# Performance work log

Hardware: AMD Instinct MI355X
Metric: run time of the kernel (lower is better)

Reference implementation:

```python
import math
import jax, jax.numpy as jnp
import numpy as np

T, C, NH = 2048, 1024, 16
HD = C // NH


def setup_inputs() -> dict:
    key = jax.random.key(0)
    ks = jax.random.split(key, 5)
    return {
        "x": jax.random.normal(ks[0], (T, C), dtype=jnp.float32),
        "w_attn": jax.random.normal(ks[1], (3 * C, C), dtype=jnp.float32) * (1.0 / math.sqrt(C)),
        "b_attn": jax.random.normal(ks[2], (3 * C,), dtype=jnp.float32) * 0.02,
        "w_proj": jax.random.normal(ks[3], (C, C), dtype=jnp.float32) * (1.0 / math.sqrt(C)),
        "b_proj": jax.random.normal(ks[4], (C,), dtype=jnp.float32) * 0.02,
    }


def reference(x, w_attn, b_attn, w_proj, b_proj):
    t, c = x.shape
    # qkv projection: eqx Linear computes W @ x + b, vmapped over T
    qkv = x @ w_attn.T + b_attn  # (T, 3C)
    q, k, v = jnp.split(qkv, 3, axis=1)  # each (T, C)
    # (T, NH, HD) -> (NH, T, HD)
    q = jnp.swapaxes(q.reshape(t, NH, HD), 0, 1)
    k = jnp.swapaxes(k.reshape(t, NH, HD), 0, 1)
    v = jnp.swapaxes(v.reshape(t, NH, HD), 0, 1)
    att = jnp.einsum('hqd,hkd->hqk', q, k) / math.sqrt(HD)  # (NH, T, T)
    causal = jnp.tril(jnp.ones((t, t), dtype=bool))
    att = jnp.where(causal[None, :, :], att, -jnp.inf)
    att = jax.nn.softmax(att, axis=-1)
    y = jnp.matmul(att, v)  # (NH, T, HD)
    # Faithful to source: swapaxes(1,2) on (NH, T, HD) -> (NH, HD, T), then reshape
    y = jnp.swapaxes(y, 1, 2).reshape(t, c)
    return y @ w_proj.T + b_proj
```

## Files before the change

### kernel.cpp

```cpp
#include <hip/hip_runtime.h>
#include <hip/hip_bf16.h>
#include <stdint.h>

typedef __bf16 bf16;
typedef __bf16 bf16x8 __attribute__((ext_vector_type(8)));
typedef __bf16 bf16x4 __attribute__((ext_vector_type(4)));
typedef float floatx4 __attribute__((ext_vector_type(4)));

#define T_DIM 2048
#define C_DIM 1024
#define NH    16
#define HD    64

__device__ __forceinline__ void gload_lds16(const void* g, void* l) {
    __builtin_amdgcn_global_load_lds(
        (__attribute__((address_space(1))) void*)(g),
        (__attribute__((address_space(3))) void*)(l),
        16, 0, 0);
}

#define MFMA16(a, b, c) __builtin_amdgcn_mfma_f32_16x16x32_bf16(a, b, c, 0, 0, 0)

__global__ __launch_bounds__(256) void cvt_all(
    const float* __restrict__ x, const float* __restrict__ wa,
    const float* __restrict__ wp,
    bf16* __restrict__ xb, bf16* __restrict__ wab, bf16* __restrict__ wpb)
{
    const int i = blockIdx.x * 256 + threadIdx.x;
    const float* src; bf16* dst; int off;
    if (i < 262144)      { src = x;  dst = xb;  off = i; }
    else if (i < 655360) { src = wa; dst = wab; off = i - 262144; }
    else                 { src = wp; dst = wpb; off = i - 655360; }
    const float4 a = ((const float4*)src)[off * 2];
    const float4 b = ((const float4*)src)[off * 2 + 1];
    bf16x8 o;
    o[0] = (bf16)a.x; o[1] = (bf16)a.y; o[2] = (bf16)a.z; o[3] = (bf16)a.w;
    o[4] = (bf16)b.x; o[5] = (bf16)b.y; o[6] = (bf16)b.z; o[7] = (bf16)b.w;
    *(bf16x8*)(dst + (size_t)off * 8) = o;
}

template<int MODE, int TN>
__global__ __launch_bounds__(256) void csa_gemm_bt(
    const bf16* __restrict__ A, const bf16* __restrict__ B,
    const float* __restrict__ bias,
    void* __restrict__ out0v, bf16* __restrict__ out1, bf16* __restrict__ out2)
{
    constexpr int K = 1024;
    constexpr int MT = (TN == 128) ? 4 : 2;
    __shared__ __align__(16) bf16 sA[128 * 32];
    __shared__ __align__(16) bf16 sB[TN * 32];

    const int tid  = threadIdx.x;
    const int lane = tid & 63;
    const int wid  = tid >> 6;
    const int rowbase = (TN == 128) ? (wid & 1) * 64 : wid * 32;
    const int colbase = (TN == 128) ? (wid >> 1) * 64 : 0;
    const int tileM = blockIdx.x * 128;
    const int tileN = blockIdx.y * TN;

    const int r0 = tid >> 2;
    const int c0 = (tid & 3) * 8;
    const long aBase = (long)(tileM + r0) * K + c0;
    const long bBase = (long)(tileN + r0) * K + c0;

    const int fr   = lane & 15;
    const int quad = lane >> 4;
    const int fc   = quad * 8;

    floatx4 acc[MT][4];
#pragma unroll
    for (int i = 0; i < MT; i++)
#pragma unroll
        for (int j = 0; j < 4; j++) acc[i][j] = (floatx4){0.f, 0.f, 0.f, 0.f};

    for (int k0 = 0; k0 < K; k0 += 32) {
        __syncthreads();
        gload_lds16(A + aBase + k0,                 sA + tid * 8);
        gload_lds16(A + aBase + (long)64 * K + k0,  sA + 2048 + tid * 8);
        gload_lds16(B + bBase + k0,                 sB + tid * 8);
        if (TN == 128)
            gload_lds16(B + bBase + (long)64 * K + k0, sB + 2048 + tid * 8);
        __syncthreads();

        bf16x8 af[MT], bfr[4];
#pragma unroll
        for (int mt = 0; mt < MT; mt++)
            af[mt] = *(const bf16x8*)(sA + (rowbase + mt * 16 + fr) * 32 + fc);
#pragma unroll
        for (int nt = 0; nt < 4; nt++)
            bfr[nt] = *(const bf16x8*)(sB + (colbase + nt * 16 + fr) * 32 + fc);
#pragma unroll
        for (int mt = 0; mt < MT; mt++)
#pragma unroll
            for (int nt = 0; nt < 4; nt++)
                acc[mt][nt] = MFMA16(af[mt], bfr[nt], acc[mt][nt]);
    }

#pragma unroll
    for (int mt = 0; mt < MT; mt++) {
#pragma unroll
        for (int nt = 0; nt < 4; nt++) {
            const int gn = tileN + colbase + nt * 16 + fr;
            const float bv = bias[gn];
            const int gmb = tileM + rowbase + mt * 16 + quad * 4;
            if (MODE == 0) {
                const int which = gn >> 10;
                const int w2 = gn & 1023;
                const int hh = w2 >> 6, d = w2 & 63;
                if (which == 2) {
                    bf16x4 pk;
#pragma unroll
                    for (int r = 0; r < 4; r++) pk[r] = (bf16)(acc[mt][nt][r] + bv);
                    *(bf16x4*)(out2 + ((long)(hh * HD + d) << 11) + gmb) = pk;
                } else {
                    bf16* dst = (which == 0) ? (bf16*)out0v : out1;
#pragma unroll
                    for (int r = 0; r < 4; r++)
                        dst[((long)hh * T_DIM + gmb + r) * HD + d] =
                            (bf16)(acc[mt][nt][r] + bv);
                }
            } else {
#pragma unroll
                for (int r = 0; r < 4; r++)
                    ((float*)out0v)[(long)(gmb + r) * C_DIM + gn] =
                        acc[mt][nt][r] + bv;
            }
        }
    }
}

__global__ __launch_bounds__(256) void csa_attn_chunk(
    const bf16* __restrict__ Qh, const bf16* __restrict__ Kh,
    const bf16* __restrict__ Vth, float* __restrict__ Opart,
    float* __restrict__ lpart, bf16* __restrict__ YY)
{
    __shared__ __align__(16) bf16 sK[2][64 * 64];
    __shared__ __align__(16) bf16 sV[2][64 * 64];
    __shared__ __align__(16) bf16 sP[4][16 * 64];

    const int c  = blockIdx.x;
    const int h  = blockIdx.y;
    const int qt = 31 - (int)blockIdx.z;
    const int nk = qt + 1;
    const int kt0 = c * 8;
    if (kt0 >= nk) return;
    const int ktend = (kt0 + 8 < nk) ? kt0 + 8 : nk;

    const int tid  = threadIdx.x;
    const int lane = tid & 63;
    const int wid  = tid >> 6;
    const int fr   = lane & 15;
    const int quad = lane >> 4;
    const int f7   = fr & 7;
    const int q0   = qt * 64;
    const int qg   = q0 + wid * 16 + fr;

    const bf16* qrow = Qh + ((long)h * T_DIM + qg) * HD;
    const bf16x8 qf0 = *(const bf16x8*)(qrow + quad * 8);
    const bf16x8 qf1 = *(const bf16x8*)(qrow + quad * 8 + 32);

    const int rb   = tid >> 3;
    const int cswz = (tid & 7) ^ (rb & 7);

    auto stage = [&](int b, int k0) {
        gload_lds16(Kh + ((long)(h * T_DIM + k0 + rb) << 6) + cswz * 8,
                    &sK[b][0] + tid * 8);
        gload_lds16(Kh + ((long)(h * T_DIM + k0 + rb + 32) << 6) + cswz * 8,
                    &sK[b][0] + 2048 + tid * 8);
        gload_lds16(Vth + ((long)(h * HD + rb) << 11) + k0 + cswz * 8,
                    &sV[b][0] + tid * 8);
        gload_lds16(Vth + ((long)(h * HD + rb + 32) << 11) + k0 + cswz * 8,
                    &sV[b][0] + 2048 + tid * 8);
    };

    stage(0, kt0 * 64);

    float l_i = 0.f;
    floatx4 o_acc[4];
#pragma unroll
    for (int d4 = 0; d4 < 4; d4++) o_acc[d4] = (floatx4){0.f, 0.f, 0.f, 0.f};

    for (int kt = kt0; kt < ktend; ++kt) {
        const int it = kt - kt0;
        __syncthreads();
        if (kt + 1 < ktend) stage((it + 1) & 1, (kt + 1) * 64);
        const bf16* K_ = &sK[it & 1][0];
        const bf16* V_ = &sV[it & 1][0];
        const int k0 = kt * 64;
        const bool diag = (kt == qt);

        float p[4][4];
#pragma unroll
        for (int nt = 0; nt < 4; nt++) {
            const bf16* kr = K_ + (nt * 16 + fr) * 64;
            const bf16x8 ka0 = *(const bf16x8*)(kr + (quad ^ f7) * 8);
            const bf16x8 ka1 = *(const bf16x8*)(kr + ((quad + 4) ^ f7) * 8);
            floatx4 z = (floatx4){0.f, 0.f, 0.f, 0.f};
            z = MFMA16(ka0, qf0, z);
            z = MFMA16(ka1, qf1, z);
            const int kgb = k0 + nt * 16 + quad * 4;
#pragma unroll
            for (int r = 0; r < 4; r++) {
                const float e = __builtin_amdgcn_exp2f(z[r] * 0.1803368801f);
                p[nt][r] = (!diag || (kgb + r <= qg)) ? e : 0.f;
            }
        }

        float s = 0.f;
#pragma unroll
        for (int nt = 0; nt < 4; nt++)
#pragma unroll
            for (int r = 0; r < 4; r++) s += p[nt][r];
        s += __shfl_xor(s, 16);
        s += __shfl_xor(s, 32);
        l_i += s;

        bf16* pw = &sP[wid][0];
#pragma unroll
        for (int nt = 0; nt < 4; nt++) {
            bf16x4 pk;
#pragma unroll
            for (int r = 0; r < 4; r++) pk[r] = (bf16)p[nt][r];
            *(bf16x4*)(pw + fr * 64 +
                       (((2 * nt + (quad >> 1)) ^ f7) * 8) + (quad & 1) * 4) = pk;
        }
        asm volatile("s_waitcnt lgkmcnt(0)" ::: "memory");
        const bf16x8 pa0 = *(const bf16x8*)(pw + fr * 64 + (quad ^ f7) * 8);
        const bf16x8 pa1 = *(const bf16x8*)(pw + fr * 64 + ((quad + 4) ^ f7) * 8);

#pragma unroll
        for (int d4 = 0; d4 < 4; d4++) {
            const bf16* vr = V_ + (d4 * 16 + fr) * 64;
            const bf16x8 vb0 = *(const bf16x8*)(vr + (quad ^ f7) * 8);
            const bf16x8 vb1 = *(const bf16x8*)(vr + ((quad + 4) ^ f7) * 8);
            o_acc[d4] = MFMA16(pa0, vb0, o_acc[d4]);
            o_acc[d4] = MFMA16(pa1, vb1, o_acc[d4]);
        }
    }

    if (kt0 == 0 && ktend == nk) {
        const float inv_self = 1.f / l_i;
        float inv[4];
#pragma unroll
        for (int r = 0; r < 4; r++) inv[r] = __shfl(inv_self, quad * 4 + r);
#pragma unroll
        for (int r = 0; r < 4; r++) {
            const int q = q0 + wid * 16 + quad * 4 + r;
            const int rq = q >> 10, cq = q & 1023;
#pragma unroll
            for (int d4 = 0; d4 < 4; d4++) {
                const int d = d4 * 16 + fr;
                YY[(long)(h * 128 + 2 * d + rq) * 1024 + cq] =
                    (bf16)(o_acc[d4][r] * inv[r]);
            }
        }
    } else {
        const long obase = ((long)((h * 32 + qt) * 4 + c)) * 4096;
#pragma unroll
        for (int d4 = 0; d4 < 4; d4++)
#pragma unroll
            for (int r = 0; r < 4; r++)
                Opart[obase + (wid * 16 + quad * 4 + r) * 64 + d4 * 16 + fr] =
                    o_acc[d4][r];
        if (quad == 0)
            lpart[((h * 32 + qt) * 4 + c) * 64 + wid * 16 + fr] = l_i;
    }
}

__global__ __launch_bounds__(256) void csa_combine(
    const float* __restrict__ Opart, const float* __restrict__ lpart,
    bf16* __restrict__ YY)
{
    const int qt = blockIdx.x + 8;
    const int h  = blockIdx.y;
    const int nc = (qt >> 3) + 1;
    const int t  = threadIdx.x;
    const int q  = t >> 2;
    const int d0 = (t & 3) * 16;

    const long obase = ((long)((h * 32 + qt) * 4)) * 4096 + q * 64 + d0;
    const int  lbase = (h * 32 + qt) * 4 * 64 + q;

    float4 acc[4] = {};
    float lq = 0.f;
    for (int c = 0; c < nc; c++) {
        const float4* src = (const float4*)(Opart + obase + (long)c * 4096);
#pragma unroll
        for (int j = 0; j < 4; j++) {
            const float4 v = src[j];
            acc[j].x += v.x; acc[j].y += v.y; acc[j].z += v.z; acc[j].w += v.w;
        }
        lq += lpart[lbase + c * 64];
    }
    const float inv = 1.f / lq;
    const int qglob = qt * 64 + q;
    const int rq = qglob >> 10, cq = qglob & 1023;
#pragma unroll
    for (int j = 0; j < 4; j++) {
        const float vv[4] = {acc[j].x, acc[j].y, acc[j].z, acc[j].w};
#pragma unroll
        for (int k = 0; k < 4; k++) {
            const int d = d0 + j * 4 + k;
            YY[(long)(h * 128 + 2 * d + rq) * 1024 + cq] = (bf16)(vv[k] * inv);
        }
    }
}

extern "C" void kernel_launch(void* const* d_in, const int* in_sizes, int n_in,
                              void* d_out, int out_size, void* d_ws, size_t ws_size,
                              hipStream_t stream) {
    (void)in_sizes; (void)n_in; (void)out_size; (void)ws_size;
    const float* x      = (const float*)d_in[0];
    const float* w_attn = (const float*)d_in[1];
    const float* b_attn = (const float*)d_in[2];
    const float* w_proj = (const float*)d_in[3];
    const float* b_proj = (const float*)d_in[4];

    bf16* xb  = (bf16*)d_ws;
    bf16* wab = xb  + (size_t)T_DIM * C_DIM;
    bf16* wpb = wab + (size_t)3 * C_DIM * C_DIM;
    bf16* Q   = wpb + (size_t)C_DIM * C_DIM;
    bf16* Kp  = Q   + (size_t)NH * T_DIM * HD;
    bf16* Vt  = Kp  + (size_t)NH * T_DIM * HD;
    bf16* YY  = Vt  + (size_t)NH * T_DIM * HD;
    float* Opart = (float*)(YY + (size_t)T_DIM * C_DIM);
    float* lpart = Opart + (size_t)16 * 32 * 4 * 4096;

    cvt_all<<<3072, 256, 0, stream>>>(x, w_attn, w_proj, xb, wab, wpb);

    csa_gemm_bt<0, 64><<<dim3(16, 48), 256, 0, stream>>>(xb, wab, b_attn, Q, Kp, Vt);
    csa_attn_chunk<<<dim3(4, NH, 32), 256, 0, stream>>>(Q, Kp, Vt, Opart, lpart, YY);
    csa_combine<<<dim3(24, NH), 256, 0, stream>>>(Opart, lpart, YY);
    csa_gemm_bt<1, 64><<<dim3(16, 16), 256, 0, stream>>>(YY, wpb, b_proj, d_out, nullptr, nullptr);
}
```

Measured before the change: 152.0 us.

## Split attention key tile across waves and reduce partial outputs through LDS

```diff
diff --git a/kernel.cpp b/kernel.cpp
--- a/kernel.cpp
+++ b/kernel.cpp
@@ -6,6 +6,7 @@
 typedef __bf16 bf16x8 __attribute__((ext_vector_type(8)));
 typedef __bf16 bf16x4 __attribute__((ext_vector_type(4)));
 typedef float floatx4 __attribute__((ext_vector_type(4)));
+typedef short short4v __attribute__((ext_vector_type(4)));
 
 #define T_DIM 2048
 #define C_DIM 1024
@@ -19,7 +20,8 @@
         16, 0, 0);
 }
 
-#define MFMA16(a, b, c) __builtin_amdgcn_mfma_f32_16x16x32_bf16(a, b, c, 0, 0, 0)
+#define MFMA16(a, b, c)  __builtin_amdgcn_mfma_f32_16x16x32_bf16(a, b, c, 0, 0, 0)
+#define MFMAK16(a, b, c) __builtin_amdgcn_mfma_f32_16x16x16bf16_1k(a, b, c, 0, 0, 0)
 
 __global__ __launch_bounds__(256) void cvt_all(
     const float* __restrict__ x, const float* __restrict__ wa,
@@ -134,9 +136,13 @@
     const bf16* __restrict__ Vth, float* __restrict__ Opart,
     float* __restrict__ lpart, bf16* __restrict__ YY)
 {
-    __shared__ __align__(16) bf16 sK[2][64 * 64];
-    __shared__ __align__(16) bf16 sV[2][64 * 64];
-    __shared__ __align__(16) bf16 sP[4][16 * 64];
+    __shared__ __align__(16) char smem[41984];
+    bf16* sK0 = (bf16*)(smem);
+    bf16* sK1 = (bf16*)(smem + 8192);
+    bf16* sV0 = (bf16*)(smem + 16384);
+    bf16* sV1 = (bf16*)(smem + 24576);
+    float* sR = (float*)smem;
+    float* sL = (float*)(smem + 40960);
 
     const int c  = blockIdx.x;
     const int h  = blockIdx.y;
@@ -153,117 +159,172 @@
     const int quad = lane >> 4;
     const int f7   = fr & 7;
     const int q0   = qt * 64;
-    const int qg   = q0 + wid * 16 + fr;
-
-    const bf16* qrow = Qh + ((long)h * T_DIM + qg) * HD;
-    const bf16x8 qf0 = *(const bf16x8*)(qrow + quad * 8);
-    const bf16x8 qf1 = *(const bf16x8*)(qrow + quad * 8 + 32);
+
+    bf16x8 qf[4][2];
+#pragma unroll
+    for (int g = 0; g < 4; g++) {
+        const bf16* qrow = Qh + ((long)h * T_DIM + q0 + g * 16 + fr) * HD;
+        qf[g][0] = *(const bf16x8*)(qrow + quad * 8);
+        qf[g][1] = *(const bf16x8*)(qrow + quad * 8 + 32);
+    }
 
     const int rb   = tid >> 3;
     const int cswz = (tid & 7) ^ (rb & 7);
 
-    auto stage = [&](int b, int k0) {
+    auto stage = [&](bf16* sKd, bf16* sVd, int k0) {
         gload_lds16(Kh + ((long)(h * T_DIM + k0 + rb) << 6) + cswz * 8,
-                    &sK[b][0] + tid * 8);
+                    sKd + tid * 8);
         gload_lds16(Kh + ((long)(h * T_DIM + k0 + rb + 32) << 6) + cswz * 8,
-                    &sK[b][0] + 2048 + tid * 8);
+                    sKd + 2048 + tid * 8);
         gload_lds16(Vth + ((long)(h * HD + rb) << 11) + k0 + cswz * 8,
-                    &sV[b][0] + tid * 8);
+                    sVd + tid * 8);
         gload_lds16(Vth + ((long)(h * HD + rb + 32) << 11) + k0 + cswz * 8,
-                    &sV[b][0] + 2048 + tid * 8);
+                    sVd + 2048 + tid * 8);
     };
 
-    stage(0, kt0 * 64);
-
-    float l_i = 0.f;
-    floatx4 o_acc[4];
-#pragma unroll
-    for (int d4 = 0; d4 < 4; d4++) o_acc[d4] = (floatx4){0.f, 0.f, 0.f, 0.f};
+    stage(sK0, sV0, kt0 * 64);
+
+    float l_i[4] = {0.f, 0.f, 0.f, 0.f};
+    floatx4 o_acc[4][4];
+#pragma unroll
+    for (int g = 0; g < 4; g++)
+#pragma unroll
+        for (int gd = 0; gd < 4; gd++) o_acc[g][gd] = (floatx4){0.f, 0.f, 0.f, 0.f};
 
     for (int kt = kt0; kt < ktend; ++kt) {
         const int it = kt - kt0;
         __syncthreads();
-        if (kt + 1 < ktend) stage((it + 1) & 1, (kt + 1) * 64);
-        const bf16* K_ = &sK[it & 1][0];
-        const bf16* V_ = &sV[it & 1][0];
+        if (kt + 1 < ktend)
+            stage((it & 1) ? sK0 : sK1, (it & 1) ? sV0 : sV1, (kt + 1) * 64);
+        const bf16* K_ = (it & 1) ? sK1 : sK0;
+        const bf16* V_ = (it & 1) ? sV1 : sV0;
         const int k0 = kt * 64;
         const bool diag = (kt == qt);
 
-        float p[4][4];
-#pragma unroll
-        for (int nt = 0; nt < 4; nt++) {
-            const bf16* kr = K_ + (nt * 16 + fr) * 64;
-            const bf16x8 ka0 = *(const bf16x8*)(kr + (quad ^ f7) * 8);
-            const bf16x8 ka1 = *(const bf16x8*)(kr + ((quad + 4) ^ f7) * 8);
+        const bf16* kr = K_ + (wid * 16 + fr) * 64;
+        const bf16x8 ka0 = *(const bf16x8*)(kr + (quad ^ f7) * 8);
+        const bf16x8 ka1 = *(const bf16x8*)(kr + ((quad + 4) ^ f7) * 8);
+        const int kg = k0 + wid * 16 + quad * 4;
+
+        short4v pa[4];
+#pragma unroll
+        for (int g = 0; g < 4; g++) {
             floatx4 z = (floatx4){0.f, 0.f, 0.f, 0.f};
-            z = MFMA16(ka0, qf0, z);
-            z = MFMA16(ka1, qf1, z);
-            const int kgb = k0 + nt * 16 + quad * 4;
+            z = MFMA16(ka0, qf[g][0], z);
+            z = MFMA16(ka1, qf[g][1], z);
+            const int qg = q0 + g * 16 + fr;
+            bf16x4 pk;
+            float s = 0.f;
 #pragma unroll
             for (int r = 0; r < 4; r++) {
                 const float e = __builtin_amdgcn_exp2f(z[r] * 0.1803368801f);
-                p[nt][r] = (!diag || (kgb + r <= qg)) ? e : 0.f;
+                const float pv = (!diag || (kg + r <= qg)) ? e : 0.f;
+                s += pv;
+                pk[r] = (bf16)pv;
             }
-        }
-
-        float s = 0.f;
-#pragma unroll
-        for (int nt = 0; nt < 4; nt++)
-#pragma unroll
-            for (int r = 0; r < 4; r++) s += p[nt][r];
-        s += __shfl_xor(s, 16);
-        s += __shfl_xor(s, 32);
-        l_i += s;
-
-        bf16* pw = &sP[wid][0];
-#pragma unroll
-        for (int nt = 0; nt < 4; nt++) {
-            bf16x4 pk;
-#pragma unroll
-            for (int r = 0; r < 4; r++) pk[r] = (bf16)p[nt][r];
-            *(bf16x4*)(pw + fr * 64 +
-                       (((2 * nt + (quad >> 1)) ^ f7) * 8) + (quad & 1) * 4) = pk;
-        }
-        asm volatile("s_waitcnt lgkmcnt(0)" ::: "memory");
-        const bf16x8 pa0 = *(const bf16x8*)(pw + fr * 64 + (quad ^ f7) * 8);
-        const bf16x8 pa1 = *(const bf16x8*)(pw + fr * 64 + ((quad + 4) ^ f7) * 8);
-
-#pragma unroll
-        for (int d4 = 0; d4 < 4; d4++) {
-            const bf16* vr = V_ + (d4 * 16 + fr) * 64;
-            const bf16x8 vb0 = *(const bf16x8*)(vr + (quad ^ f7) * 8);
-            const bf16x8 vb1 = *(const bf16x8*)(vr + ((quad + 4) ^ f7) * 8);
-            o_acc[d4] = MFMA16(pa0, vb0, o_acc[d4]);
-            o_acc[d4] = MFMA16(pa1, vb1, o_acc[d4]);
-        }
-    }
+            s += __shfl_xor(s, 16);
+            s += __shfl_xor(s, 32);
+            l_i[g] += s;
+            pa[g] = __builtin_bit_cast(short4v, pk);
+        }
+
+        const int vchunk = ((wid * 2 + (quad >> 1)) ^ f7) * 8 + (quad & 1) * 4;
+#pragma unroll
+        for (int gd = 0; gd < 4; gd++) {
+            const bf16* vrow = V_ + (gd * 16 + fr) * 64;
+            const short4v vbs = __builtin_bit_cast(short4v,
+                                    *(const bf16x4*)(vrow + vchunk));
+#pragma unroll
+            for (int g = 0; g < 4; g++)
+                o_acc[g][gd] = MFMAK16(pa[g], vbs, o_acc[g][gd]);
+        }
+    }
+
+    __syncthreads();
+    if (quad == 0) {
+#pragma unroll
+        for (int g = 0; g < 4; g++) sL[wid * 64 + g * 16 + fr] = l_i[g];
+    }
+    const int side = wid >> 1;
+#pragma unroll
+    for (int g = 0; g < 4; g++) {
+        if ((g >> 1) != side) {
+            float* R = sR + (wid * 2 + (g & 1)) * 1280;
+#pragma unroll
+            for (int gd = 0; gd < 4; gd++)
+                *(floatx4*)(R + (gd * 16 + fr) * 20 + quad * 4) = o_acc[g][gd];
+        }
+    }
+    __syncthreads();
+#pragma unroll
+    for (int g = 0; g < 4; g++) {
+        if ((g >> 1) == side) {
+            const float* R = sR + ((wid ^ 2) * 2 + (g & 1)) * 1280;
+#pragma unroll
+            for (int gd = 0; gd < 4; gd++)
+                o_acc[g][gd] += *(const floatx4*)(R + (gd * 16 + fr) * 20 + quad * 4);
+        }
+    }
+    __syncthreads();
+#pragma unroll
+    for (int g = 0; g < 4; g++) {
+        if (g == (wid ^ 1)) {
+            float* R = sR + wid * 1280;
+#pragma unroll
+            for (int gd = 0; gd < 4; gd++)
+                *(floatx4*)(R + (gd * 16 + fr) * 20 + quad * 4) = o_acc[g][gd];
+        }
+    }
+    __syncthreads();
+#pragma unroll
+    for (int g = 0; g < 4; g++) {
+        if (g == wid) {
+            const float* R = sR + (wid ^ 1) * 1280;
+#pragma unroll
+            for (int gd = 0; gd < 4; gd++)
+                o_acc[g][gd] += *(const floatx4*)(R + (gd * 16 + fr) * 20 + quad * 4);
+        }
+    }
+
+    const float lf = sL[0 * 64 + wid * 16 + fr] + sL[1 * 64 + wid * 16 + fr] +
+                     sL[2 * 64 + wid * 16 + fr] + sL[3 * 64 + wid * 16 + fr];
 
     if (kt0 == 0 && ktend == nk) {
-        const float inv_self = 1.f / l_i;
+        const float inv_self = 1.f / lf;
         float inv[4];
 #pragma unroll
         for (int r = 0; r < 4; r++) inv[r] = __shfl(inv_self, quad * 4 + r);
 #pragma unroll
-        for (int r = 0; r < 4; r++) {
-            const int q = q0 + wid * 16 + quad * 4 + r;
-            const int rq = q >> 10, cq = q & 1023;
-#pragma unroll
-            for (int d4 = 0; d4 < 4; d4++) {
-                const int d = d4 * 16 + fr;
-                YY[(long)(h * 128 + 2 * d + rq) * 1024 + cq] =
-                    (bf16)(o_acc[d4][r] * inv[r]);
+        for (int g = 0; g < 4; g++) {
+            if (g == wid) {
+#pragma unroll
+                for (int r = 0; r < 4; r++) {
+                    const int q = q0 + g * 16 + quad * 4 + r;
+                    const int rq = q >> 10, cq = q & 1023;
+#pragma unroll
+                    for (int gd = 0; gd < 4; gd++) {
+                        const int d = gd * 16 + fr;
+                        YY[(long)(h * 128 + 2 * d + rq) * 1024 + cq] =
+                            (bf16)(o_acc[g][gd][r] * inv[r]);
+                    }
+                }
             }
         }
     } else {
         const long obase = ((long)((h * 32 + qt) * 4 + c)) * 4096;
 #pragma unroll
-        for (int d4 = 0; d4 < 4; d4++)
-#pragma unroll
-            for (int r = 0; r < 4; r++)
-                Opart[obase + (wid * 16 + quad * 4 + r) * 64 + d4 * 16 + fr] =
-                    o_acc[d4][r];
+        for (int g = 0; g < 4; g++) {
+            if (g == wid) {
+#pragma unroll
+                for (int gd = 0; gd < 4; gd++)
+#pragma unroll
+                    for (int r = 0; r < 4; r++)
+                        Opart[obase + (g * 16 + quad * 4 + r) * 64 + gd * 16 + fr] =
+                            o_acc[g][gd][r];
+            }
+        }
         if (quad == 0)
-            lpart[((h * 32 + qt) * 4 + c) * 64 + wid * 16 + fr] = l_i;
+            lpart[((h * 32 + qt) * 4 + c) * 64 + wid * 16 + fr] = lf;
     }
 }
 
```

New measurement: 167.6 us. 10.2% more time.

## Feed softmax probabilities to PV MFMA directly from registers, dropping LDS round-trip

Applied to the files above, without the earlier changes.

```diff
diff --git a/kernel.cpp b/kernel.cpp
--- a/kernel.cpp
+++ b/kernel.cpp
@@ -6,6 +6,7 @@
 typedef __bf16 bf16x8 __attribute__((ext_vector_type(8)));
 typedef __bf16 bf16x4 __attribute__((ext_vector_type(4)));
 typedef float floatx4 __attribute__((ext_vector_type(4)));
+typedef short short4v __attribute__((ext_vector_type(4)));
 
 #define T_DIM 2048
 #define C_DIM 1024
@@ -19,7 +20,8 @@
         16, 0, 0);
 }
 
-#define MFMA16(a, b, c) __builtin_amdgcn_mfma_f32_16x16x32_bf16(a, b, c, 0, 0, 0)
+#define MFMA16(a, b, c)  __builtin_amdgcn_mfma_f32_16x16x32_bf16(a, b, c, 0, 0, 0)
+#define MFMAK16(a, b, c) __builtin_amdgcn_mfma_f32_16x16x16bf16_1k(a, b, c, 0, 0, 0)
 
 __global__ __launch_bounds__(256) void cvt_all(
     const float* __restrict__ x, const float* __restrict__ wa,
@@ -136,7 +138,6 @@
 {
     __shared__ __align__(16) bf16 sK[2][64 * 64];
     __shared__ __align__(16) bf16 sV[2][64 * 64];
-    __shared__ __align__(16) bf16 sP[4][16 * 64];
 
     const int c  = blockIdx.x;
     const int h  = blockIdx.y;
@@ -189,7 +190,8 @@
         const int k0 = kt * 64;
         const bool diag = (kt == qt);
 
-        float p[4][4];
+        short4v pa[4];
+        float s = 0.f;
 #pragma unroll
         for (int nt = 0; nt < 4; nt++) {
             const bf16* kr = K_ + (nt * 16 + fr) * 64;
@@ -199,42 +201,30 @@
             z = MFMA16(ka0, qf0, z);
             z = MFMA16(ka1, qf1, z);
             const int kgb = k0 + nt * 16 + quad * 4;
+            bf16x4 pk;
 #pragma unroll
             for (int r = 0; r < 4; r++) {
                 const float e = __builtin_amdgcn_exp2f(z[r] * 0.1803368801f);
-                p[nt][r] = (!diag || (kgb + r <= qg)) ? e : 0.f;
+                const float pv = (!diag || (kgb + r <= qg)) ? e : 0.f;
+                s += pv;
+                pk[r] = (bf16)pv;
             }
-        }
-
-        float s = 0.f;
-#pragma unroll
-        for (int nt = 0; nt < 4; nt++)
-#pragma unroll
-            for (int r = 0; r < 4; r++) s += p[nt][r];
+            pa[nt] = __builtin_bit_cast(short4v, pk);
+        }
         s += __shfl_xor(s, 16);
         s += __shfl_xor(s, 32);
         l_i += s;
 
-        bf16* pw = &sP[wid][0];
-#pragma unroll
-        for (int nt = 0; nt < 4; nt++) {
-            bf16x4 pk;
-#pragma unroll
-            for (int r = 0; r < 4; r++) pk[r] = (bf16)p[nt][r];
-            *(bf16x4*)(pw + fr * 64 +
-                       (((2 * nt + (quad >> 1)) ^ f7) * 8) + (quad & 1) * 4) = pk;
-        }
-        asm volatile("s_waitcnt lgkmcnt(0)" ::: "memory");
-        const bf16x8 pa0 = *(const bf16x8*)(pw + fr * 64 + (quad ^ f7) * 8);
-        const bf16x8 pa1 = *(const bf16x8*)(pw + fr * 64 + ((quad + 4) ^ f7) * 8);
-
 #pragma unroll
         for (int d4 = 0; d4 < 4; d4++) {
-            const bf16* vr = V_ + (d4 * 16 + fr) * 64;
-            const bf16x8 vb0 = *(const bf16x8*)(vr + (quad ^ f7) * 8);
-            const bf16x8 vb1 = *(const bf16x8*)(vr + ((quad + 4) ^ f7) * 8);
-            o_acc[d4] = MFMA16(pa0, vb0, o_acc[d4]);
-            o_acc[d4] = MFMA16(pa1, vb1, o_acc[d4]);
+            const bf16* vrow = V_ + (d4 * 16 + fr) * 64;
+#pragma unroll
+            for (int nt = 0; nt < 4; nt++) {
+                const short4v vb = __builtin_bit_cast(short4v,
+                    *(const bf16x4*)(vrow +
+                        (((2 * nt + (quad >> 1)) ^ f7) * 8) + (quad & 1) * 4));
+                o_acc[d4] = MFMAK16(pa[nt], vb, o_acc[d4]);
+            }
         }
     }
 
```

New measurement: 155.3 us. 2.1% more time.
